# Kernel optimization log

Measured on AMD Instinct MI355X. Metric: run time of the kernel, lower is better.

The kernel has to match this reference:

```python
import jax, jax.numpy as jnp
import numpy as np

N_QUBITS = 4
DIM = 16
N_QLAYERS = 2

def _cnot_perm(c, t):
    idx = np.arange(DIM)
    cbit = (idx >> (N_QUBITS - 1 - c)) & 1
    return np.where(cbit == 1, idx ^ (1 << (N_QUBITS - 1 - t)), idx)

# ring entanglement: CNOT(0,1), CNOT(1,2), CNOT(2,3), CNOT(3,0)
RING_PERMS = [jnp.asarray(_cnot_perm(i, (i + 1) % N_QUBITS)) for i in range(N_QUBITS)]
_idx = np.arange(DIM)
ZSIGNS = jnp.asarray(np.stack([1.0 - 2.0 * ((_idx >> (N_QUBITS - 1 - q)) & 1) for q in range(N_QUBITS)], axis=1).astype(np.float32))  # (16, 4)

def _rx(t):
    c = jnp.cos(t / 2).astype(jnp.complex64)
    s = jnp.sin(t / 2).astype(jnp.complex64)
    return jnp.stack([jnp.stack([c, -1j * s]), jnp.stack([-1j * s, c])])

def _ry(t):
    c = jnp.cos(t / 2).astype(jnp.complex64)
    s = jnp.sin(t / 2).astype(jnp.complex64)
    return jnp.stack([jnp.stack([c, -s]), jnp.stack([s, c])])

def _rz(t):
    e = jnp.exp(-0.5j * t.astype(jnp.complex64))
    z = jnp.zeros((), jnp.complex64)
    return jnp.stack([jnp.stack([e, z]), jnp.stack([z, jnp.conj(e)])])

def _apply_1q(state, g, q):
    # wire 0 is the most significant bit (PennyLane convention)
    s = state.reshape(2 ** q, 2, 2 ** (N_QUBITS - 1 - q))
    return jnp.einsum('ij,ajc->aic', g, s).reshape(DIM)

def _circuit(angles, qw):
    # angles: (4,), qw: (n_qlayers, 4, 3); returns PauliZ expvals (4,)
    state = jnp.zeros(DIM, jnp.complex64).at[0].set(1.0)
    for q in range(N_QUBITS):
        state = _apply_1q(state, _ry(angles[q]), q)
    for l in range(N_QLAYERS):
        for q in range(N_QUBITS):
            state = _apply_1q(state, _rx(qw[l, q, 0]), q)
            state = _apply_1q(state, _ry(qw[l, q, 1]), q)
            state = _apply_1q(state, _rz(qw[l, q, 2]), q)
        for p in RING_PERMS:
            state = state[p]
    probs = jnp.abs(state) ** 2
    return probs @ ZSIGNS

def _conv(x, w, b, stride, pad):
    y = jax.lax.conv_general_dilated(x, w, (stride, stride), [(pad, pad), (pad, pad)], dimension_numbers=('NCHW', 'OIHW', 'NCHW'))
    return y + b[None, :, None, None]

def _bn(x, g, b, m, v):
    scale = (g / jnp.sqrt(v + 1e-5))[None, :, None, None]
    return (x - m[None, :, None, None]) * scale + b[None, :, None, None]

def _forward(x, c1w, c1b, bn1g, bn1b, bn1m, bn1v, c2w, c2b, bn2g, bn2b, bn2m, bn2v, c3w, c3b, bn3g, bn3b, bn3m, bn3v, pre_w, pre_b, qw, pw1, pb1, pw2, pb2):
    B = x.shape[0]
    h = jax.nn.relu(_bn(_conv(x, c1w, c1b, 4, 3), bn1g, bn1b, bn1m, bn1v))   # (B,32,56,56)
    h = jax.nn.relu(_bn(_conv(h, c2w, c2b, 2, 1), bn2g, bn2b, bn2m, bn2v))   # (B,64,28,28)
    h = jax.nn.relu(_bn(_conv(h, c3w, c3b, 2, 1), bn3g, bn3b, bn3m, bn3v))   # (B,128,14,14)
    h = h.reshape(B, 128, 2, 7, 2, 7).mean(axis=(3, 5))                       # AdaptiveAvgPool2d((2,2))
    f = h.reshape(B, 128 * 4)
    ang = jnp.tanh(f @ pre_w.T + pre_b) * jnp.pi                              # (B,4)
    qout = jax.vmap(lambda a: _circuit(a, qw))(ang)                            # (B,4) batched statevector sim
    h1 = jax.nn.relu(qout @ pw1.T + pb1)                                       # dropout inactive (eval)
    return h1 @ pw2.T + pb2

def setup_inputs() -> dict:
    key = jax.random.key(0)
    ks = jax.random.split(key, 16)
    d = {
        'x': jax.random.normal(ks[0], (128, 3, 224, 224), jnp.float32),
        'c1w': jax.random.normal(ks[1], (32, 3, 7, 7), jnp.float32) * 0.05,
        'c1b': jax.random.normal(ks[2], (32,), jnp.float32) * 0.05,
        'bn1g': jnp.ones((32,), jnp.float32), 'bn1b': jnp.zeros((32,), jnp.float32),
        'bn1m': jnp.zeros((32,), jnp.float32), 'bn1v': jnp.ones((32,), jnp.float32),
        'c2w': jax.random.normal(ks[3], (64, 32, 3, 3), jnp.float32) * 0.05,
        'c2b': jax.random.normal(ks[4], (64,), jnp.float32) * 0.05,
        'bn2g': jnp.ones((64,), jnp.float32), 'bn2b': jnp.zeros((64,), jnp.float32),
        'bn2m': jnp.zeros((64,), jnp.float32), 'bn2v': jnp.ones((64,), jnp.float32),
        'c3w': jax.random.normal(ks[5], (128, 64, 3, 3), jnp.float32) * 0.05,
        'c3b': jax.random.normal(ks[6], (128,), jnp.float32) * 0.05,
        'bn3g': jnp.ones((128,), jnp.float32), 'bn3b': jnp.zeros((128,), jnp.float32),
        'bn3m': jnp.zeros((128,), jnp.float32), 'bn3v': jnp.ones((128,), jnp.float32),
        'pre_w': jax.random.normal(ks[7], (4, 512), jnp.float32) * 0.04,
        'pre_b': jax.random.normal(ks[8], (4,), jnp.float32) * 0.04,
        'qw': jax.random.normal(ks[9], (2, 4, 3), jnp.float32) * 0.1,
        'pw1': jax.random.normal(ks[10], (64, 4), jnp.float32) * 0.5,
        'pb1': jax.random.normal(ks[11], (64,), jnp.float32) * 0.5,
        'pw2': jax.random.normal(ks[12], (5, 64), jnp.float32) * 0.12,
        'pb2': jax.random.normal(ks[13], (5,), jnp.float32) * 0.12,
    }
    return d

def reference(x, c1w, c1b, bn1g, bn1b, bn1m, bn1v, c2w, c2b, bn2g, bn2b, bn2m, bn2v, c3w, c3b, bn3g, bn3b, bn3m, bn3v, pre_w, pre_b, qw, pw1, pb1, pw2, pb2):
    return _forward(x, c1w, c1b, bn1g, bn1b, bn1m, bn1v, c2w, c2b, bn2g, bn2b, bn2m, bn2v, c3w, c3b, bn3g, bn3b, bn3m, bn3v, pre_w, pre_b, qw, pw1, pb1, pw2, pb2)
```

## Files before the change

kernel.cpp:

```cpp
#include <hip/hip_runtime.h>
#include <math.h>

#define DEV __device__ __forceinline__

typedef __attribute__((ext_vector_type(8))) __bf16 bf16x8;
typedef __attribute__((ext_vector_type(4))) float f32x4;

__global__ void prep_all(
    const float* __restrict__ x, long nx,
    const float* __restrict__ c1w, const float* __restrict__ c1b,
    const float* __restrict__ g1, const float* __restrict__ b1,
    const float* __restrict__ m1, const float* __restrict__ v1,
    const float* __restrict__ c2w, const float* __restrict__ c2b,
    const float* __restrict__ g2, const float* __restrict__ b2,
    const float* __restrict__ m2, const float* __restrict__ v2,
    const float* __restrict__ c3w, const float* __restrict__ c3b,
    const float* __restrict__ g3, const float* __restrict__ b3,
    const float* __restrict__ m3, const float* __restrict__ v3,
    __bf16* __restrict__ xpad,
    __bf16* __restrict__ wb1, __bf16* __restrict__ wb2, __bf16* __restrict__ wb3,
    float* __restrict__ sc1, float* __restrict__ sh1,
    float* __restrict__ sc2, float* __restrict__ sh2,
    float* __restrict__ sc3, float* __restrict__ sh3)
{
    long gid = (long)blockIdx.x * 256 + threadIdx.x;
    long gs = (long)gridDim.x * 256;
    for (long e = gid; e < nx; e += gs) xpad[e] = (__bf16)x[e];

    for (long e = gid; e < 32 * 192; e += gs) {
        int oc = e / 192, k = e % 192, rr = k >> 3, kw = k & 7;
        wb1[e] = (rr < 21 && kw < 7) ? (__bf16)c1w[oc * 147 + rr * 7 + kw] : (__bf16)0.f;
    }
    for (long e = gid; e < 64 * 384; e += gs) {
        int oc = e / 384, k = e % 384, rr = k >> 2, kw = k & 3;
        wb2[e] = (kw < 3) ? (__bf16)c2w[oc * 288 + rr * 3 + kw] : (__bf16)0.f;
    }
    for (long e = gid; e < 128 * 768; e += gs) {
        int oc = e / 768, k = e % 768, rr = k >> 2, kw = k & 3;
        wb3[e] = (kw < 3) ? (__bf16)c3w[oc * 576 + rr * 3 + kw] : (__bf16)0.f;
    }
    if (gid < 32) {
        float s = g1[gid] * rsqrtf(v1[gid] + 1e-5f);
        sc1[gid] = s; sh1[gid] = (c1b[gid] - m1[gid]) * s + b1[gid];
    } else if (gid < 96) {
        int i = gid - 32;
        float s = g2[i] * rsqrtf(v2[i] + 1e-5f);
        sc2[i] = s; sh2[i] = (c2b[i] - m2[i]) * s + b2[i];
    } else if (gid < 224) {
        int i = gid - 96;
        float s = g3[i] * rsqrtf(v3[i] + 1e-5f);
        sc3[i] = s; sh3[i] = (c3b[i] - m3[i]) * s + b3[i];
    }
}

template<typename OUTT, int IC, int KS, int RW, int S, int P,
         int IH, int IW, int OH, int OW, int OC, int KTP, int KOFF, int KCH,
         bool EPI>
__global__ __launch_bounds__(256, 6) void conv_mfma_kernel(
    const __bf16* __restrict__ xo,
    const __bf16* __restrict__ wb,
    const float* __restrict__ scale,
    const float* __restrict__ shift,
    OUTT* __restrict__ out)
{
    constexpr int KITER = KCH / 32;
    static_assert(KCH % 32 == 0, "KCH");
    constexpr int OHW = OH * OW;
    constexpr int IHW = IH * IW;
    constexpr int LDR = 40;
    constexpr int NROW = 16 / RW;
    constexpr int RU = RW / 2;

    __shared__ __attribute__((aligned(16))) __bf16 Is[128 * LDR];
    __shared__ __attribute__((aligned(16))) __bf16 Ws[32 * LDR];

    const int tid = threadIdx.x;
    const int sb0 = blockIdx.x * 128;
    const int oc0 = blockIdx.y * 32;

    const int sm = tid & 127;
    const int kpb = tid >> 7;
    int a_n, a_ih0, a_iw0;
    {
        int m = sb0 + sm;
        a_n = m / OHW;
        int rem = m % OHW;
        a_ih0 = (rem / OW) * S - P;
        a_iw0 = (rem % OW) * S - P;
    }
    unsigned ihok = 0;
    #pragma unroll
    for (int t = 0; t < KS; ++t)
        ihok |= (unsigned)(((a_ih0 + t) >= 0) && ((a_ih0 + t) < IH)) << t;
    const int iwlow = a_iw0 < 0 ? -a_iw0 : 0;
    const __bf16* xp = xo + ((size_t)a_n * IC * IHW + (ptrdiff_t)a_ih0 * IW + a_iw0);

    const int w_oc = tid >> 2;
    const int w_j  = tid & 3;

    const int wave = tid >> 6, lane = tid & 63;
    const int quad = lane >> 4, l16 = lane & 15;

    f32x4 acc[2][2] = {};

    #pragma unroll
    for (int ci = 0; ci < KITER; ++ci) {
        const int k0 = KOFF + ci * 32;

        union { unsigned u[8]; bf16x8 v[2]; } Pk;
        #pragma unroll
        for (int half = 0; half < 2; ++half) {
            if (kpb == half) {
                #pragma unroll
                for (int r = 0; r < NROW; ++r) {
                    const int rr = (k0 / RW) + half * NROW + r;
                    if (rr >= IC * KS) {
                        #pragma unroll
                        for (int q = 0; q < RU; ++q) Pk.u[r * RU + q] = 0u;
                    } else {
                        const int ic = rr / KS, kh = rr % KS;
                        const unsigned* rp =
                            (const unsigned*)(xp + (ic * IHW + kh * IW));
                        unsigned t[RU];
                        #pragma unroll
                        for (int q = 0; q < RU; ++q) t[q] = rp[q];
                        bool rok = (ihok >> kh) & 1u;
                        #pragma unroll
                        for (int q = 0; q < RU; ++q) t[q] = rok ? t[q] : 0u;
                        #pragma unroll
                        for (int j = 0; j < P; ++j) {
                            unsigned msk = (j & 1) ? 0x0000FFFFu : 0xFFFF0000u;
                            t[j >> 1] = (j < iwlow) ? (t[j >> 1] & msk) : t[j >> 1];
                        }
                        #pragma unroll
                        for (int q = 0; q < RU; ++q) Pk.u[r * RU + q] = t[q];
                    }
                }
            }
        }
        bf16x8 wv = {};
        if (tid < 128)
            wv = *(const bf16x8*)&wb[(size_t)(oc0 + w_oc) * KTP + k0 + w_j * 8];

        __syncthreads();
        *(bf16x8*)&Is[sm * LDR + kpb * 16]     = Pk.v[0];
        *(bf16x8*)&Is[sm * LDR + kpb * 16 + 8] = Pk.v[1];
        if (tid < 128) *(bf16x8*)&Ws[w_oc * LDR + w_j * 8] = wv;
        __syncthreads();

        bf16x8 afr[2], bfr[2];
        #pragma unroll
        for (int mt = 0; mt < 2; ++mt)
            afr[mt] = *(const bf16x8*)&Ws[(mt * 16 + l16) * LDR + quad * 8];
        #pragma unroll
        for (int nt = 0; nt < 2; ++nt)
            bfr[nt] = *(const bf16x8*)&Is[(wave * 32 + nt * 16 + l16) * LDR + quad * 8];
        #pragma unroll
        for (int mt = 0; mt < 2; ++mt)
            #pragma unroll
            for (int nt = 0; nt < 2; ++nt)
                acc[mt][nt] = __builtin_amdgcn_mfma_f32_16x16x32_bf16(
                    afr[mt], bfr[nt], acc[mt][nt], 0, 0, 0);
    }

    #pragma unroll
    for (int mt = 0; mt < 2; ++mt) {
        #pragma unroll
        for (int r = 0; r < 4; ++r) {
            int oc = oc0 + mt * 16 + quad * 4 + r;
            float scl = EPI ? scale[oc] : 0.f;
            float shf = EPI ? shift[oc] : 0.f;
            #pragma unroll
            for (int nt = 0; nt < 2; ++nt) {
                int sg = sb0 + wave * 32 + nt * 16 + l16;
                int n = sg / OHW, s = sg % OHW;
                float v = acc[mt][nt][r];
                if (EPI) {
                    v = fmaf(v, scl, shf);
                    v = v > 0.f ? v : 0.f;
                }
                out[((size_t)n * OC + oc) * OHW + s] = (OUTT)v;
            }
        }
    }
}

__global__ __launch_bounds__(256) void pool_bn_kernel(
    const float* __restrict__ p3a, const float* __restrict__ p3b,
    const float* __restrict__ sc3, const float* __restrict__ sh3,
    float* __restrict__ f)
{
    int idx = blockIdx.x * 256 + threadIdx.x;
    int b = idx >> 9, p = idx & 511;
    int c = p >> 2, i = (p >> 1) & 1, j = p & 1;
    size_t base = ((size_t)b * 128 + c) * 196 + (i * 7) * 14 + j * 7;
    float scl = sc3[c], shf = sh3[c];
    float s = 0.f;
    #pragma unroll
    for (int u = 0; u < 7; ++u)
        #pragma unroll
        for (int v = 0; v < 7; ++v) {
            size_t k = base + u * 14 + v;
            float val = fmaf(p3a[k] + p3b[k], scl, shf);
            s += val > 0.f ? val : 0.f;
        }
    f[idx] = s * (1.f / 49.f);
}

DEV void gate_ry(float* re, float* im, int q, float th) {
    float c = cosf(th * 0.5f), s = sinf(th * 0.5f);
    int mask = 8 >> q;
    for (int i = 0; i < 16; ++i) {
        if (i & mask) continue;
        int j = i | mask;
        float r0 = re[i], i0 = im[i], r1 = re[j], i1 = im[j];
        re[i] = c * r0 - s * r1;  im[i] = c * i0 - s * i1;
        re[j] = s * r0 + c * r1;  im[j] = s * i0 + c * i1;
    }
}
DEV void gate_rx(float* re, float* im, int q, float th) {
    float c = cosf(th * 0.5f), s = sinf(th * 0.5f);
    int mask = 8 >> q;
    for (int i = 0; i < 16; ++i) {
        if (i & mask) continue;
        int j = i | mask;
        float r0 = re[i], i0 = im[i], r1 = re[j], i1 = im[j];
        re[i] = c * r0 + s * i1;  im[i] = c * i0 - s * r1;
        re[j] = s * i0 + c * r1;  im[j] = -s * r0 + c * i1;
    }
}
DEV void gate_rz(float* re, float* im, int q, float th) {
    float c = cosf(th * 0.5f), s = sinf(th * 0.5f);
    int mask = 8 >> q;
    for (int i = 0; i < 16; ++i) {
        float sg = (i & mask) ? s : -s;
        float r = re[i], m = im[i];
        re[i] = c * r - sg * m;
        im[i] = c * m + sg * r;
    }
}
DEV void gate_cnot(float* re, float* im, int c, int t) {
    int cm = 8 >> c, tm = 8 >> t;
    for (int i = 0; i < 16; ++i) {
        if ((i & cm) && !(i & tm)) {
            int j = i | tm;
            float r = re[i]; re[i] = re[j]; re[j] = r;
            float m = im[i]; im[i] = im[j]; im[j] = m;
        }
    }
}

__global__ __launch_bounds__(256) void head_kernel(
    const float* __restrict__ fpool,
    const float* __restrict__ pre_w, const float* __restrict__ pre_b,
    const float* __restrict__ qw,
    const float* __restrict__ pw1, const float* __restrict__ pb1,
    const float* __restrict__ pw2, const float* __restrict__ pb2,
    float* __restrict__ out)
{
    __shared__ float f[512];
    __shared__ float ang[4];
    __shared__ float sre[16], simg[16];
    __shared__ float zexp[4];
    __shared__ float h1[64];

    int b = blockIdx.x;
    int t = threadIdx.x;

    for (int p = t; p < 512; p += 256) f[p] = fpool[b * 512 + p];
    __syncthreads();

    int wv = t >> 6, lane = t & 63;
    float partial = 0.f;
    for (int d = lane; d < 512; d += 64)
        partial += f[d] * pre_w[wv * 512 + d];
    #pragma unroll
    for (int off = 32; off > 0; off >>= 1)
        partial += __shfl_down(partial, off, 64);
    if (lane == 0)
        ang[wv] = tanhf(partial + pre_b[wv]) * 3.14159265358979323846f;
    __syncthreads();

    if (t == 0) {
        for (int i = 0; i < 16; ++i) { sre[i] = 0.f; simg[i] = 0.f; }
        sre[0] = 1.f;
        for (int q = 0; q < 4; ++q) gate_ry(sre, simg, q, ang[q]);
        for (int l = 0; l < 2; ++l) {
            for (int q = 0; q < 4; ++q) {
                const float* qq = qw + (l * 4 + q) * 3;
                gate_rx(sre, simg, q, qq[0]);
                gate_ry(sre, simg, q, qq[1]);
                gate_rz(sre, simg, q, qq[2]);
            }
            gate_cnot(sre, simg, 0, 1);
            gate_cnot(sre, simg, 1, 2);
            gate_cnot(sre, simg, 2, 3);
            gate_cnot(sre, simg, 3, 0);
        }
        for (int q = 0; q < 4; ++q) {
            float z = 0.f;
            for (int i = 0; i < 16; ++i) {
                float p2 = sre[i] * sre[i] + simg[i] * simg[i];
                z += (((i >> (3 - q)) & 1) ? -p2 : p2);
            }
            zexp[q] = z;
        }
    }
    __syncthreads();

    if (t < 64) {
        float s = pb1[t];
        #pragma unroll
        for (int k = 0; k < 4; ++k) s += zexp[k] * pw1[t * 4 + k];
        h1[t] = s > 0.f ? s : 0.f;
    }
    __syncthreads();

    if (t < 5) {
        float s = pb2[t];
        for (int k = 0; k < 64; ++k) s += h1[k] * pw2[t * 64 + k];
        out[b * 5 + t] = s;
    }
}

extern "C" void kernel_launch(void* const* d_in, const int* in_sizes, int n_in,
                              void* d_out, int out_size, void* d_ws, size_t ws_size,
                              hipStream_t stream) {
    const float* x    = (const float*)d_in[0];
    const float* c1w  = (const float*)d_in[1];
    const float* c1b  = (const float*)d_in[2];
    const float* bn1g = (const float*)d_in[3];
    const float* bn1b = (const float*)d_in[4];
    const float* bn1m = (const float*)d_in[5];
    const float* bn1v = (const float*)d_in[6];
    const float* c2w  = (const float*)d_in[7];
    const float* c2b  = (const float*)d_in[8];
    const float* bn2g = (const float*)d_in[9];
    const float* bn2b = (const float*)d_in[10];
    const float* bn2m = (const float*)d_in[11];
    const float* bn2v = (const float*)d_in[12];
    const float* c3w  = (const float*)d_in[13];
    const float* c3bi = (const float*)d_in[14];
    const float* bn3g = (const float*)d_in[15];
    const float* bn3b = (const float*)d_in[16];
    const float* bn3m = (const float*)d_in[17];
    const float* bn3v = (const float*)d_in[18];
    const float* prw  = (const float*)d_in[19];
    const float* prb  = (const float*)d_in[20];
    const float* qw   = (const float*)d_in[21];
    const float* pw1  = (const float*)d_in[22];
    const float* pb1  = (const float*)d_in[23];
    const float* pw2  = (const float*)d_in[24];
    const float* pb2  = (const float*)d_in[25];

    const int N = in_sizes[0] / (3 * 224 * 224);
    const long NX  = (long)N * 3 * 224 * 224;
    const size_t NC1 = (size_t)N * 32 * 56 * 56;
    const size_t NC2 = (size_t)N * 64 * 28 * 28;

    __bf16* ws_h = (__bf16*)d_ws;
    __bf16* xpad_alloc = ws_h;
    __bf16* xpad_o = xpad_alloc + 1023;
    __bf16* c1o_alloc = xpad_alloc + NX + 2048;
    __bf16* c1o_o = c1o_alloc + 63;
    __bf16* c2o_alloc = c1o_alloc + NC1 + 128;
    __bf16* c2o_o = c2o_alloc + 63;
    __bf16* wb1 = c2o_alloc + NC2 + 128;
    __bf16* wb2 = wb1 + 32 * 192;
    __bf16* wb3 = wb2 + 64 * 384;
    float* sc1 = (float*)(wb3 + 128 * 768);
    float* sh1 = sc1 + 32;
    float* sc2 = sh1 + 32;  float* sh2 = sc2 + 64;
    float* sc3 = sh2 + 64;  float* sh3 = sc3 + 128;
    float* fpool = sh3 + 128;
    float* p3a = (float*)xpad_alloc;
    float* p3b = p3a + (size_t)N * 128 * 14 * 14;

    prep_all<<<1024, 256, 0, stream>>>(
        x, NX,
        c1w, c1b, bn1g, bn1b, bn1m, bn1v,
        c2w, c2b, bn2g, bn2b, bn2m, bn2v,
        c3w, c3bi, bn3g, bn3b, bn3m, bn3v,
        xpad_o, wb1, wb2, wb3, sc1, sh1, sc2, sh2, sc3, sh3);

    conv_mfma_kernel<__bf16, 3, 7, 8, 4, 3, 224, 224, 56, 56, 32, 192, 0, 192, true>
        <<<dim3(401408 / 128, 1), 256, 0, stream>>>(xpad_o, wb1, sc1, sh1, c1o_o);
    conv_mfma_kernel<__bf16, 32, 3, 4, 2, 1, 56, 56, 28, 28, 64, 384, 0, 384, true>
        <<<dim3(100352 / 128, 2), 256, 0, stream>>>(c1o_o, wb2, sc2, sh2, c2o_o);
    conv_mfma_kernel<float, 64, 3, 4, 2, 1, 28, 28, 14, 14, 128, 768, 0, 384, false>
        <<<dim3(25088 / 128, 4), 256, 0, stream>>>(c2o_o, wb3, sc3, sh3, p3a);
    conv_mfma_kernel<float, 64, 3, 4, 2, 1, 28, 28, 14, 14, 128, 768, 384, 384, false>
        <<<dim3(25088 / 128, 4), 256, 0, stream>>>(c2o_o, wb3, sc3, sh3, p3b);

    pool_bn_kernel<<<(N * 512) / 256, 256, 0, stream>>>(p3a, p3b, sc3, sh3, fpool);
    head_kernel<<<N, 256, 0, stream>>>(fpool, prw, prb, qw,
                                       pw1, pb1, pw2, pb2, (float*)d_out);
}
```

Before: 269.0 us.

## Vectorize input cast, shift conv padding into weights, merge conv3 split launches

The fp32-to-bf16 input conversion now loads two float4 values and writes one 8-wide bf16 vector per thread, so each thread handles eight elements instead of one. The padded weight layouts are shifted by one column and the input pointer starts one element earlier. This keeps the 32-bit row loads aligned and reduces left-edge masking to a single boolean instead of a per-column loop. The two K-half conv3 launches become one launch with a z dimension, and the per-half branch in the patch gather is removed. The risk is correctness at the shifted edges, since the leftmost extra element is now read and must be zeroed by the weights or the mask.

Result: faster. 250.9 us (-6.7%).

```diff
diff --git a/kernel.cpp b/kernel.cpp
--- a/kernel.cpp
+++ b/kernel.cpp
@@ -7,7 +7,7 @@
 typedef __attribute__((ext_vector_type(4))) float f32x4;
 
 __global__ void prep_all(
-    const float* __restrict__ x, long nx,
+    const float* __restrict__ x, long nx8,
     const float* __restrict__ c1w, const float* __restrict__ c1b,
     const float* __restrict__ g1, const float* __restrict__ b1,
     const float* __restrict__ m1, const float* __restrict__ v1,
@@ -25,19 +25,28 @@
 {
     long gid = (long)blockIdx.x * 256 + threadIdx.x;
     long gs = (long)gridDim.x * 256;
-    for (long e = gid; e < nx; e += gs) xpad[e] = (__bf16)x[e];
+    const float4* x4 = (const float4*)x;
+    bf16x8* xp8 = (bf16x8*)xpad;
+    for (long e = gid; e < nx8; e += gs) {
+        float4 a = x4[2 * e], b = x4[2 * e + 1];
+        bf16x8 o;
+        o[0] = (__bf16)a.x; o[1] = (__bf16)a.y; o[2] = (__bf16)a.z; o[3] = (__bf16)a.w;
+        o[4] = (__bf16)b.x; o[5] = (__bf16)b.y; o[6] = (__bf16)b.z; o[7] = (__bf16)b.w;
+        xp8[e] = o;
+    }
 
     for (long e = gid; e < 32 * 192; e += gs) {
         int oc = e / 192, k = e % 192, rr = k >> 3, kw = k & 7;
-        wb1[e] = (rr < 21 && kw < 7) ? (__bf16)c1w[oc * 147 + rr * 7 + kw] : (__bf16)0.f;
+        wb1[e] = (rr < 21 && kw >= 1) ? (__bf16)c1w[oc * 147 + rr * 7 + kw - 1]
+                                      : (__bf16)0.f;
     }
     for (long e = gid; e < 64 * 384; e += gs) {
         int oc = e / 384, k = e % 384, rr = k >> 2, kw = k & 3;
-        wb2[e] = (kw < 3) ? (__bf16)c2w[oc * 288 + rr * 3 + kw] : (__bf16)0.f;
+        wb2[e] = (kw >= 1) ? (__bf16)c2w[oc * 288 + rr * 3 + kw - 1] : (__bf16)0.f;
     }
     for (long e = gid; e < 128 * 768; e += gs) {
         int oc = e / 768, k = e % 768, rr = k >> 2, kw = k & 3;
-        wb3[e] = (kw < 3) ? (__bf16)c3w[oc * 576 + rr * 3 + kw] : (__bf16)0.f;
+        wb3[e] = (kw >= 1) ? (__bf16)c3w[oc * 576 + rr * 3 + kw - 1] : (__bf16)0.f;
     }
     if (gid < 32) {
         float s = g1[gid] * rsqrtf(v1[gid] + 1e-5f);
@@ -56,12 +65,13 @@
 template<typename OUTT, int IC, int KS, int RW, int S, int P,
          int IH, int IW, int OH, int OW, int OC, int KTP, int KOFF, int KCH,
          bool EPI>
-__global__ __launch_bounds__(256, 6) void conv_mfma_kernel(
+DEV void conv_body(
     const __bf16* __restrict__ xo,
     const __bf16* __restrict__ wb,
     const float* __restrict__ scale,
     const float* __restrict__ shift,
-    OUTT* __restrict__ out)
+    OUTT* __restrict__ out,
+    __bf16* Is, __bf16* Ws)
 {
     constexpr int KITER = KCH / 32;
     static_assert(KCH % 32 == 0, "KCH");
@@ -70,9 +80,6 @@
     constexpr int LDR = 40;
     constexpr int NROW = 16 / RW;
     constexpr int RU = RW / 2;
-
-    __shared__ __attribute__((aligned(16))) __bf16 Is[128 * LDR];
-    __shared__ __attribute__((aligned(16))) __bf16 Ws[32 * LDR];
 
     const int tid = threadIdx.x;
     const int sb0 = blockIdx.x * 128;
@@ -92,8 +99,9 @@
     #pragma unroll
     for (int t = 0; t < KS; ++t)
         ihok |= (unsigned)(((a_ih0 + t) >= 0) && ((a_ih0 + t) < IH)) << t;
-    const int iwlow = a_iw0 < 0 ? -a_iw0 : 0;
-    const __bf16* xp = xo + ((size_t)a_n * IC * IHW + (ptrdiff_t)a_ih0 * IW + a_iw0);
+    const bool left = (a_iw0 < 0);
+    const __bf16* xp = xo + ((size_t)a_n * IC * IHW + (ptrdiff_t)a_ih0 * IW
+                             + (a_iw0 - 1));
 
     const int w_oc = tid >> 2;
     const int w_j  = tid & 3;
@@ -109,33 +117,24 @@
 
         union { unsigned u[8]; bf16x8 v[2]; } Pk;
         #pragma unroll
-        for (int half = 0; half < 2; ++half) {
-            if (kpb == half) {
+        for (int r = 0; r < NROW; ++r) {
+            const int rr = (k0 / RW) + kpb * NROW + r;
+            if (rr >= IC * KS) {
                 #pragma unroll
-                for (int r = 0; r < NROW; ++r) {
-                    const int rr = (k0 / RW) + half * NROW + r;
-                    if (rr >= IC * KS) {
-                        #pragma unroll
-                        for (int q = 0; q < RU; ++q) Pk.u[r * RU + q] = 0u;
-                    } else {
-                        const int ic = rr / KS, kh = rr % KS;
-                        const unsigned* rp =
-                            (const unsigned*)(xp + (ic * IHW + kh * IW));
-                        unsigned t[RU];
-                        #pragma unroll
-                        for (int q = 0; q < RU; ++q) t[q] = rp[q];
-                        bool rok = (ihok >> kh) & 1u;
-                        #pragma unroll
-                        for (int q = 0; q < RU; ++q) t[q] = rok ? t[q] : 0u;
-                        #pragma unroll
-                        for (int j = 0; j < P; ++j) {
-                            unsigned msk = (j & 1) ? 0x0000FFFFu : 0xFFFF0000u;
-                            t[j >> 1] = (j < iwlow) ? (t[j >> 1] & msk) : t[j >> 1];
-                        }
-                        #pragma unroll
-                        for (int q = 0; q < RU; ++q) Pk.u[r * RU + q] = t[q];
-                    }
-                }
+                for (int q = 0; q < RU; ++q) Pk.u[r * RU + q] = 0u;
+            } else {
+                const int ic = rr / KS, kh = rr % KS;
+                const unsigned* rp = (const unsigned*)(xp + (ic * IHW + kh * IW));
+                unsigned t[RU];
+                #pragma unroll
+                for (int q = 0; q < RU; ++q) t[q] = rp[q];
+                bool rok = (ihok >> kh) & 1u;
+                #pragma unroll
+                for (int q = 0; q < RU; ++q) t[q] = rok ? t[q] : 0u;
+                t[0] = left ? (t[0] & 0x0000FFFFu) : t[0];
+                if constexpr (P >= 2) t[1] = left ? 0u : t[1];
+                #pragma unroll
+                for (int q = 0; q < RU; ++q) Pk.u[r * RU + q] = t[q];
             }
         }
         bf16x8 wv = {};
@@ -183,6 +182,33 @@
             }
         }
     }
+}
+
+template<typename OUTT, int IC, int KS, int RW, int S, int P,
+         int IH, int IW, int OH, int OW, int OC, int KTP, int KCH, bool EPI>
+__global__ __launch_bounds__(256, 6) void conv_mfma_kernel(
+    const __bf16* __restrict__ xo, const __bf16* __restrict__ wb,
+    const float* __restrict__ scale, const float* __restrict__ shift,
+    OUTT* __restrict__ out)
+{
+    __shared__ __attribute__((aligned(16))) __bf16 Is[128 * 40];
+    __shared__ __attribute__((aligned(16))) __bf16 Ws[32 * 40];
+    conv_body<OUTT, IC, KS, RW, S, P, IH, IW, OH, OW, OC, KTP, 0, KCH, EPI>(
+        xo, wb, scale, shift, out, Is, Ws);
+}
+
+__global__ __launch_bounds__(256, 6) void conv3_kernel(
+    const __bf16* __restrict__ xo, const __bf16* __restrict__ wb,
+    float* __restrict__ p3a, float* __restrict__ p3b)
+{
+    __shared__ __attribute__((aligned(16))) __bf16 Is[128 * 40];
+    __shared__ __attribute__((aligned(16))) __bf16 Ws[32 * 40];
+    if (blockIdx.z == 0)
+        conv_body<float, 64, 3, 4, 2, 1, 28, 28, 14, 14, 128, 768, 0, 384, false>(
+            xo, wb, nullptr, nullptr, p3a, Is, Ws);
+    else
+        conv_body<float, 64, 3, 4, 2, 1, 28, 28, 14, 14, 128, 768, 384, 384, false>(
+            xo, wb, nullptr, nullptr, p3b, Is, Ws);
 }
 
 __global__ __launch_bounds__(256) void pool_bn_kernel(
@@ -360,12 +386,12 @@
 
     __bf16* ws_h = (__bf16*)d_ws;
     __bf16* xpad_alloc = ws_h;
-    __bf16* xpad_o = xpad_alloc + 1023;
-    __bf16* c1o_alloc = xpad_alloc + NX + 2048;
-    __bf16* c1o_o = c1o_alloc + 63;
-    __bf16* c2o_alloc = c1o_alloc + NC1 + 128;
-    __bf16* c2o_o = c2o_alloc + 63;
-    __bf16* wb1 = c2o_alloc + NC2 + 128;
+    __bf16* xpad = xpad_alloc + 1024;
+    __bf16* c1o_alloc = xpad_alloc + 1024 + NX + 64;
+    __bf16* c1o = c1o_alloc + 64;
+    __bf16* c2o_alloc = c1o_alloc + 64 + NC1 + 64;
+    __bf16* c2o = c2o_alloc + 64;
+    __bf16* wb1 = c2o_alloc + 64 + NC2 + 64;
     __bf16* wb2 = wb1 + 32 * 192;
     __bf16* wb3 = wb2 + 64 * 384;
     float* sc1 = (float*)(wb3 + 128 * 768);
@@ -377,20 +403,17 @@
     float* p3b = p3a + (size_t)N * 128 * 14 * 14;
 
     prep_all<<<1024, 256, 0, stream>>>(
-        x, NX,
+        x, NX / 8,
         c1w, c1b, bn1g, bn1b, bn1m, bn1v,
         c2w, c2b, bn2g, bn2b, bn2m, bn2v,
         c3w, c3bi, bn3g, bn3b, bn3m, bn3v,
-        xpad_o, wb1, wb2, wb3, sc1, sh1, sc2, sh2, sc3, sh3);
-
-    conv_mfma_kernel<__bf16, 3, 7, 8, 4, 3, 224, 224, 56, 56, 32, 192, 0, 192, true>
-        <<<dim3(401408 / 128, 1), 256, 0, stream>>>(xpad_o, wb1, sc1, sh1, c1o_o);
-    conv_mfma_kernel<__bf16, 32, 3, 4, 2, 1, 56, 56, 28, 28, 64, 384, 0, 384, true>
-        <<<dim3(100352 / 128, 2), 256, 0, stream>>>(c1o_o, wb2, sc2, sh2, c2o_o);
-    conv_mfma_kernel<float, 64, 3, 4, 2, 1, 28, 28, 14, 14, 128, 768, 0, 384, false>
-        <<<dim3(25088 / 128, 4), 256, 0, stream>>>(c2o_o, wb3, sc3, sh3, p3a);
-    conv_mfma_kernel<float, 64, 3, 4, 2, 1, 28, 28, 14, 14, 128, 768, 384, 384, false>
-        <<<dim3(25088 / 128, 4), 256, 0, stream>>>(c2o_o, wb3, sc3, sh3, p3b);
+        xpad, wb1, wb2, wb3, sc1, sh1, sc2, sh2, sc3, sh3);
+
+    conv_mfma_kernel<__bf16, 3, 7, 8, 4, 3, 224, 224, 56, 56, 32, 192, 192, true>
+        <<<dim3(401408 / 128, 1), 256, 0, stream>>>(xpad, wb1, sc1, sh1, c1o);
+    conv_mfma_kernel<__bf16, 32, 3, 4, 2, 1, 56, 56, 28, 28, 64, 384, 384, true>
+        <<<dim3(100352 / 128, 2), 256, 0, stream>>>(c1o, wb2, sc2, sh2, c2o);
+    conv3_kernel<<<dim3(25088 / 128, 4, 2), 256, 0, stream>>>(c2o, wb3, p3a, p3b);
 
     pool_bn_kernel<<<(N * 512) / 256, 256, 0, stream>>>(p3a, p3b, sc3, sh3, fpool);
     head_kernel<<<N, 256, 0, stream>>>(fpool, prw, prb, qw,
```
